# Optimization experiments

Hardware: AMD Instinct MI355X
Metric: run time of the kernel (lower is better)

Reference implementation:

```python
import jax, jax.numpy as jnp
import numpy as np

B, N, D, K = 32, 8192, 128, 64
EPS_NORM = 1e-12   # F.normalize eps
EPS_COS = 1e-8     # F.cosine_similarity eps


def _l2norm(x, eps):
    n = jnp.sqrt(jnp.sum(x * x, axis=-1, keepdims=True))
    return x / jnp.maximum(n, eps)


def setup_inputs() -> dict:
    key = jax.random.key(0)
    k1, k2, k3 = jax.random.split(key, 3)
    return {
        "modal1": jax.random.normal(k1, (B, D), dtype=jnp.float32),
        "modal2": jax.random.normal(k2, (B, N, D), dtype=jnp.float32),
        "weights": jax.random.normal(k3, (B, K), dtype=jnp.float32),
    }


def reference(modal1, modal2, weights):
    # F.normalize(dim=-1)
    m1 = _l2norm(modal1, EPS_NORM)              # [B, D]
    m2 = _l2norm(modal2, EPS_NORM)              # [B, N, D]
    # F.cosine_similarity re-normalizes (eps=1e-8); idempotent here but faithful
    m1c = _l2norm(m1, EPS_COS)
    m2c = _l2norm(m2, EPS_COS)
    cos_sim = jnp.einsum("bd,bnd->bn", m1c, m2c)   # [B, N]
    _, topk_idx = jax.lax.top_k(cos_sim, K)        # [B, K]
    # gather selected normalized vectors from m2
    selected = jnp.take_along_axis(m2, topk_idx[:, :, None], axis=1)  # [B, K, D]
    w = jax.nn.softmax(weights, axis=1)            # [B, K]
    return jnp.sum(selected * w[:, :, None], axis=1)  # [B, D]
```

## Files before the change

### kernel.cpp

```cpp
#include <hip/hip_runtime.h>
#include <math.h>

#define BB 32
#define NN 8192
#define DD 128
#define KK 64
#define NBINS 4096
#define CAP 2048

__device__ __forceinline__ unsigned monokey(float f) {
    unsigned u = __float_as_uint(f);
    return (u & 0x80000000u) ? ~u : (u | 0x80000000u);
}

__global__ __launch_bounds__(256) void cos_kernel(const float* __restrict__ modal2,
                                                  const float* __restrict__ modal1,
                                                  float* __restrict__ cos_out,
                                                  float* __restrict__ inv_out) {
    const int tid = threadIdx.x;
    const int lane = tid & 63, wid = tid >> 6;
    const int b = blockIdx.x >> 6;

    __shared__ __align__(16) float m1s[DD];
    __shared__ float red[2];

    float x = 0.f;
    if (tid < DD) {
        x = modal1[b * DD + tid];
        float s = x * x;
        #pragma unroll
        for (int off = 32; off > 0; off >>= 1) s += __shfl_xor(s, off);
        if (lane == 0) red[wid] = s;
    }
    __syncthreads();
    if (tid < DD) {
        float s1 = red[0] + red[1];
        float inv1 = 1.0f / fmaxf(sqrtf(s1), 1e-12f);
        float s2 = s1 * inv1 * inv1;
        float inv2 = 1.0f / fmaxf(sqrtf(s2), 1e-8f);
        m1s[tid] = x * (inv1 * inv2);
    }
    __syncthreads();

    const int sub = lane >> 5;
    const int c = lane & 31;
    const float4 mv = *reinterpret_cast<const float4*>(&m1s[c * 4]);
    const int pair0 = blockIdx.x * 64 + wid * 16;

    #pragma unroll 4
    for (int i = 0; i < 16; ++i) {
        int r = (pair0 + i) * 2 + sub;
        const float4 xv = *reinterpret_cast<const float4*>(modal2 + (size_t)r * DD + c * 4);
        float ss = xv.x * xv.x + xv.y * xv.y + xv.z * xv.z + xv.w * xv.w;
        float dd = xv.x * mv.x + xv.y * mv.y + xv.z * mv.z + xv.w * mv.w;
        #pragma unroll
        for (int off = 16; off > 0; off >>= 1) {
            ss += __shfl_xor(ss, off);
            dd += __shfl_xor(dd, off);
        }
        if (c == 0) {
            float inv1 = 1.0f / fmaxf(sqrtf(ss), 1e-12f);
            float s2 = ss * inv1 * inv1;
            float inv2 = 1.0f / fmaxf(sqrtf(s2), 1e-8f);
            cos_out[r] = dd * inv1 * inv2;
            inv_out[r] = inv1;
        }
    }
}

__global__ __launch_bounds__(256) void topk_kernel(const float* __restrict__ modal2,
                                                   const float* __restrict__ cos_sim,
                                                   const float* __restrict__ inv_norm,
                                                   const float* __restrict__ weights,
                                                   float* __restrict__ out) {
    const int b = blockIdx.x;
    const int tid = threadIdx.x;
    const int lane = tid & 63, wid = tid >> 6;

    __shared__ __align__(16) unsigned keys[NN];
    __shared__ unsigned bins[NBINS];
    __shared__ unsigned long long cand[CAP];
    __shared__ int cnt, thr_sh;
    __shared__ int topk_idx[KK];
    __shared__ float coef[KK];
    __shared__ __align__(16) float partial[DD];

    for (int j = tid; j < NBINS; j += 256) bins[j] = 0u;
    if (tid == 0) cnt = 0;
    const float* crow = cos_sim + (size_t)b * NN;
    #pragma unroll
    for (int j = 0; j < NN / 4 / 256; ++j) {
        int i = (tid + j * 256) * 4;
        float4 v = *reinterpret_cast<const float4*>(&crow[i]);
        uint4 kv = make_uint4(monokey(v.x), monokey(v.y), monokey(v.z), monokey(v.w));
        *reinterpret_cast<uint4*>(&keys[i]) = kv;
    }
    __syncthreads();

    #pragma unroll
    for (int j = 0; j < NN / 256; ++j) {
        int n = tid + j * 256;
        atomicAdd(&bins[keys[n] >> 20], 1u);
    }
    __syncthreads();

    if (tid < 64) {
        unsigned csum = 0;
        #pragma unroll
        for (int j = 0; j < NBINS / 64; ++j) csum += bins[tid * (NBINS / 64) + j];
        unsigned T = csum;
        #pragma unroll
        for (int off = 1; off < 64; off <<= 1) {
            unsigned t2 = __shfl_down(T, off);
            if (tid + off < 64) T += t2;
        }
        unsigned long long mk = __ballot(T >= KK);
        int Cs = 63 - __builtin_clzll(mk);
        unsigned above = (Cs < 63) ? __shfl(T, Cs + 1) : 0u;
        unsigned W = bins[Cs * (NBINS / 64) + tid];
        #pragma unroll
        for (int off = 1; off < 64; off <<= 1) {
            unsigned t2 = __shfl_down(W, off);
            if (tid + off < 64) W += t2;
        }
        unsigned long long mk2 = __ballot(above + W >= KK);
        int off2 = 63 - __builtin_clzll(mk2);
        if (tid == 0) thr_sh = Cs * (NBINS / 64) + off2;
    }
    __syncthreads();
    const int thr = thr_sh;

    #pragma unroll
    for (int j = 0; j < NN / 256; ++j) {
        int n = tid + j * 256;
        unsigned k = keys[n];
        if ((int)(k >> 20) >= thr) {
            int pos = atomicAdd(&cnt, 1);
            if (pos < CAP)
                cand[pos] = ((unsigned long long)k << 32) | (unsigned)(NN - 1 - n);
        }
    }
    __syncthreads();
    const int M = min(cnt, CAP);

    for (int i = tid; i < M; i += 256) {
        unsigned long long key = cand[i];
        int r = 0;
        for (int j = 0; j < M; ++j) r += (cand[j] > key);
        if (r < KK) topk_idx[r] = NN - 1 - (int)(key & 0xffffffffu);
    }
    __syncthreads();

    if (wid == 0) {
        float wv = weights[b * KK + lane];
        float mx = wv;
        #pragma unroll
        for (int off = 32; off > 0; off >>= 1) mx = fmaxf(mx, __shfl_xor(mx, off));
        float e = expf(wv - mx);
        float s = e;
        #pragma unroll
        for (int off = 32; off > 0; off >>= 1) s += __shfl_xor(s, off);
        float w = e / s;
        int idx = topk_idx[lane];
        coef[lane] = w * inv_norm[(size_t)b * NN + idx];
    }
    __syncthreads();

    {
        int d = tid & (DD - 1);
        int half = tid >> 7;
        const float* bbase = modal2 + (size_t)b * NN * DD;
        float acc = 0.f;
        #pragma unroll
        for (int k = 0; k < KK / 2; ++k) {
            int kk2 = half * (KK / 2) + k;
            acc += coef[kk2] * bbase[(size_t)topk_idx[kk2] * DD + d];
        }
        if (half == 0) partial[d] = acc;
        __syncthreads();
        if (half == 1) out[b * DD + d] = partial[d] + acc;
    }
}

extern "C" void kernel_launch(void* const* d_in, const int* in_sizes, int n_in,
                              void* d_out, int out_size, void* d_ws, size_t ws_size,
                              hipStream_t stream) {
    const float* modal1  = (const float*)d_in[0];
    const float* modal2  = (const float*)d_in[1];
    const float* weights = (const float*)d_in[2];
    float* out = (float*)d_out;

    char* ws = (char*)d_ws;
    float* cos_sim  = (float*)ws;
    float* inv_norm = (float*)(ws + (size_t)BB * NN * 4);

    cos_kernel<<<2048, 256, 0, stream>>>(modal2, modal1, cos_sim, inv_norm);
    topk_kernel<<<BB, 256, 0, stream>>>(modal2, cos_sim, inv_norm, weights, out);
}
```

Before: 206.5 us.

## Replace histogram threshold with per-thread-max rank threshold in top-k kernel

The cos kernel now writes monotone integer keys directly. The top-k kernel moves to 512 threads and holds 16 keys per thread in registers. It picks a threshold as the 64th largest of the per-thread maxima, which guarantees at least 64 candidates, replacing the shared-memory histogram, atomics and scan. The final gather is split four ways. Candidate count can still reach CAP=1280, and the O(M^2) rank sort over candidates stays in place.

```diff
diff --git a/kernel.cpp b/kernel.cpp
--- a/kernel.cpp
+++ b/kernel.cpp
@@ -5,8 +5,8 @@
 #define NN 8192
 #define DD 128
 #define KK 64
-#define NBINS 4096
-#define CAP 2048
+#define TPB 512
+#define CAP 1280
 
 __device__ __forceinline__ unsigned monokey(float f) {
     unsigned u = __float_as_uint(f);
@@ -15,7 +15,7 @@
 
 __global__ __launch_bounds__(256) void cos_kernel(const float* __restrict__ modal2,
                                                   const float* __restrict__ modal1,
-                                                  float* __restrict__ cos_out,
+                                                  unsigned* __restrict__ key_out,
                                                   float* __restrict__ inv_out) {
     const int tid = threadIdx.x;
     const int lane = tid & 63, wid = tid >> 6;
@@ -62,88 +62,65 @@
             float inv1 = 1.0f / fmaxf(sqrtf(ss), 1e-12f);
             float s2 = ss * inv1 * inv1;
             float inv2 = 1.0f / fmaxf(sqrtf(s2), 1e-8f);
-            cos_out[r] = dd * inv1 * inv2;
+            key_out[r] = monokey(dd * inv1 * inv2);
             inv_out[r] = inv1;
         }
     }
 }
 
-__global__ __launch_bounds__(256) void topk_kernel(const float* __restrict__ modal2,
-                                                   const float* __restrict__ cos_sim,
+__global__ __launch_bounds__(TPB) void topk_kernel(const float* __restrict__ modal2,
+                                                   const unsigned* __restrict__ keys_g,
                                                    const float* __restrict__ inv_norm,
                                                    const float* __restrict__ weights,
                                                    float* __restrict__ out) {
     const int b = blockIdx.x;
     const int tid = threadIdx.x;
-    const int lane = tid & 63, wid = tid >> 6;
 
-    __shared__ __align__(16) unsigned keys[NN];
-    __shared__ unsigned bins[NBINS];
+    __shared__ unsigned tmax_s[TPB];
     __shared__ unsigned long long cand[CAP];
-    __shared__ int cnt, thr_sh;
+    __shared__ int cnt;
+    __shared__ unsigned qs;
     __shared__ int topk_idx[KK];
     __shared__ float coef[KK];
-    __shared__ __align__(16) float partial[DD];
+    __shared__ __align__(16) float partial[4][DD];
 
-    for (int j = tid; j < NBINS; j += 256) bins[j] = 0u;
+    const uint4* krow = reinterpret_cast<const uint4*>(keys_g + (size_t)b * NN);
+    uint4 kv0 = krow[tid], kv1 = krow[tid + TPB], kv2 = krow[tid + 2 * TPB], kv3 = krow[tid + 3 * TPB];
     if (tid == 0) cnt = 0;
-    const float* crow = cos_sim + (size_t)b * NN;
-    #pragma unroll
-    for (int j = 0; j < NN / 4 / 256; ++j) {
-        int i = (tid + j * 256) * 4;
-        float4 v = *reinterpret_cast<const float4*>(&crow[i]);
-        uint4 kv = make_uint4(monokey(v.x), monokey(v.y), monokey(v.z), monokey(v.w));
-        *reinterpret_cast<uint4*>(&keys[i]) = kv;
-    }
+
+    unsigned tmax = 0u;
+    #define TM(v) tmax = max(tmax, max(max((v).x, (v).y), max((v).z, (v).w)))
+    TM(kv0); TM(kv1); TM(kv2); TM(kv3);
+    #undef TM
+    tmax_s[tid] = tmax;
     __syncthreads();
 
-    #pragma unroll
-    for (int j = 0; j < NN / 256; ++j) {
-        int n = tid + j * 256;
-        atomicAdd(&bins[keys[n] >> 20], 1u);
+    int rnk = 0;
+    for (int j = 0; j < TPB; ++j) {
+        unsigned o = tmax_s[j];
+        rnk += (o > tmax) || (o == tmax && j < tid);
     }
+    if (rnk == KK - 1) qs = tmax;
     __syncthreads();
+    const unsigned q = qs;
 
-    if (tid < 64) {
-        unsigned csum = 0;
-        #pragma unroll
-        for (int j = 0; j < NBINS / 64; ++j) csum += bins[tid * (NBINS / 64) + j];
-        unsigned T = csum;
-        #pragma unroll
-        for (int off = 1; off < 64; off <<= 1) {
-            unsigned t2 = __shfl_down(T, off);
-            if (tid + off < 64) T += t2;
+    #define EMIT(kx, nx)                                                          \
+        if ((kx) >= q) {                                                          \
+            int pos = atomicAdd(&cnt, 1);                                         \
+            if (pos < CAP)                                                        \
+                cand[pos] = ((unsigned long long)(kx) << 32) | (unsigned)(NN - 1 - (nx)); \
         }
-        unsigned long long mk = __ballot(T >= KK);
-        int Cs = 63 - __builtin_clzll(mk);
-        unsigned above = (Cs < 63) ? __shfl(T, Cs + 1) : 0u;
-        unsigned W = bins[Cs * (NBINS / 64) + tid];
-        #pragma unroll
-        for (int off = 1; off < 64; off <<= 1) {
-            unsigned t2 = __shfl_down(W, off);
-            if (tid + off < 64) W += t2;
-        }
-        unsigned long long mk2 = __ballot(above + W >= KK);
-        int off2 = 63 - __builtin_clzll(mk2);
-        if (tid == 0) thr_sh = Cs * (NBINS / 64) + off2;
-    }
-    __syncthreads();
-    const int thr = thr_sh;
-
-    #pragma unroll
-    for (int j = 0; j < NN / 256; ++j) {
-        int n = tid + j * 256;
-        unsigned k = keys[n];
-        if ((int)(k >> 20) >= thr) {
-            int pos = atomicAdd(&cnt, 1);
-            if (pos < CAP)
-                cand[pos] = ((unsigned long long)k << 32) | (unsigned)(NN - 1 - n);
-        }
-    }
+    #define EMIT4(v, j)                                   \
+        { int n0 = (tid + (j) * TPB) * 4;                 \
+          EMIT((v).x, n0); EMIT((v).y, n0 + 1);           \
+          EMIT((v).z, n0 + 2); EMIT((v).w, n0 + 3); }
+    EMIT4(kv0, 0); EMIT4(kv1, 1); EMIT4(kv2, 2); EMIT4(kv3, 3);
+    #undef EMIT4
+    #undef EMIT
     __syncthreads();
     const int M = min(cnt, CAP);
 
-    for (int i = tid; i < M; i += 256) {
+    for (int i = tid; i < M; i += TPB) {
         unsigned long long key = cand[i];
         int r = 0;
         for (int j = 0; j < M; ++j) r += (cand[j] > key);
@@ -151,8 +128,8 @@
     }
     __syncthreads();
 
-    if (wid == 0) {
-        float wv = weights[b * KK + lane];
+    if (tid < 64) {
+        float wv = weights[b * KK + tid];
         float mx = wv;
         #pragma unroll
         for (int off = 32; off > 0; off >>= 1) mx = fmaxf(mx, __shfl_xor(mx, off));
@@ -160,25 +137,25 @@
         float s = e;
         #pragma unroll
         for (int off = 32; off > 0; off >>= 1) s += __shfl_xor(s, off);
-        float w = e / s;
-        int idx = topk_idx[lane];
-        coef[lane] = w * inv_norm[(size_t)b * NN + idx];
+        coef[tid] = (e / s) * inv_norm[(size_t)b * NN + topk_idx[tid]];
     }
     __syncthreads();
 
     {
         int d = tid & (DD - 1);
-        int half = tid >> 7;
+        int qq = tid >> 7;
         const float* bbase = modal2 + (size_t)b * NN * DD;
         float acc = 0.f;
         #pragma unroll
-        for (int k = 0; k < KK / 2; ++k) {
-            int kk2 = half * (KK / 2) + k;
-            acc += coef[kk2] * bbase[(size_t)topk_idx[kk2] * DD + d];
+        for (int k = 0; k < KK / 4; ++k) {
+            int kk = qq * (KK / 4) + k;
+            acc += coef[kk] * bbase[(size_t)topk_idx[kk] * DD + d];
         }
-        if (half == 0) partial[d] = acc;
+        partial[qq][d] = acc;
         __syncthreads();
-        if (half == 1) out[b * DD + d] = partial[d] + acc;
+        if (tid < DD)
+            out[b * DD + tid] = (partial[0][tid] + partial[1][tid]) +
+                                (partial[2][tid] + partial[3][tid]);
     }
 }
 
@@ -191,9 +168,9 @@
     float* out = (float*)d_out;
 
     char* ws = (char*)d_ws;
-    float* cos_sim  = (float*)ws;
+    unsigned* keys  = (unsigned*)ws;
     float* inv_norm = (float*)(ws + (size_t)BB * NN * 4);
 
-    cos_kernel<<<2048, 256, 0, stream>>>(modal2, modal1, cos_sim, inv_norm);
-    topk_kernel<<<BB, 256, 0, stream>>>(modal2, cos_sim, inv_norm, weights, out);
+    cos_kernel<<<2048, 256, 0, stream>>>(modal2, modal1, keys, inv_norm);
+    topk_kernel<<<BB, TPB, 0, stream>>>(modal2, keys, inv_norm, weights, out);
 }
```

New measurement: 215.3 us. +4.3%, slower.
